# Performance work log

Hardware: AMD Instinct MI355X
Metric: run time of the kernel (lower is better)

## Reference

```python
import jax, jax.numpy as jnp
import numpy as np

N_NODES = 50000
N_EDGES = 800000
D_IN = 512
D_OUT = 512


def setup_inputs() -> dict:
    key = jax.random.key(0)
    k1, k2, k3, k4, k5 = jax.random.split(key, 5)
    adj_rows = jnp.sort(jax.random.randint(k1, (N_EDGES,), 0, N_NODES, dtype=jnp.int32))
    adj_cols = jax.random.randint(k2, (N_EDGES,), 0, N_NODES, dtype=jnp.int32)
    adj_vals = jax.random.uniform(k3, (N_EDGES,), dtype=jnp.float32)
    u_f = jax.random.normal(k4, (N_NODES, D_IN), dtype=jnp.float32)
    # xavier_uniform init for weight [in_feats, out_feats]
    limit = float(np.sqrt(6.0 / (D_IN + D_OUT)))
    weight = jax.random.uniform(k5, (D_IN, D_OUT), dtype=jnp.float32, minval=-limit, maxval=limit)
    return {"adj_rows": adj_rows, "adj_cols": adj_cols, "adj_vals": adj_vals,
            "u_f": u_f, "weight": weight}


def reference(adj_rows, adj_cols, adj_vals, u_f, weight):
    # dense projection: [N, d_in] @ [d_in, d_out] -> [N, d_out]
    h = u_f @ weight
    # sparse adj (COO) @ h: gather source rows, scale by edge vals, scatter-add to dest rows
    msgs = adj_vals[:, None] * h[adj_cols]              # [E, d_out]
    out = jax.ops.segment_sum(msgs, adj_rows, num_segments=N_NODES)  # [N, d_out]
    return jax.nn.relu(out)
```

## Files before the change

### kernel.cpp

```cpp
#include <hip/hip_runtime.h>
#include <cstdint>
#include <cstddef>

#define N_NODES 50000
#define N_EDGES 800000
#define D 512
#define M_PAD 50048

typedef __bf16 bf16x8 __attribute__((ext_vector_type(8)));
typedef float floatx4 __attribute__((ext_vector_type(4)));

typedef const __attribute__((address_space(1))) unsigned int* gas_u32p;
typedef __attribute__((address_space(3))) unsigned int* las_u32p;

__device__ __forceinline__ unsigned short f2bf(float f) {
    unsigned int u = __builtin_bit_cast(unsigned int, f);
    u += 0x7FFFu + ((u >> 16) & 1u);
    return (unsigned short)(u >> 16);
}
__device__ __forceinline__ float bflo(unsigned int u) {
    return __builtin_bit_cast(float, u << 16);
}
__device__ __forceinline__ float bfhi(unsigned int u) {
    return __builtin_bit_cast(float, u & 0xFFFF0000u);
}
__device__ __forceinline__ bf16x8 cvt8f(floatx4 lo, floatx4 hi) {
    bf16x8 r;
    r[0] = (__bf16)lo[0]; r[1] = (__bf16)lo[1]; r[2] = (__bf16)lo[2]; r[3] = (__bf16)lo[3];
    r[4] = (__bf16)hi[0]; r[5] = (__bf16)hi[1]; r[6] = (__bf16)hi[2]; r[7] = (__bf16)hi[3];
    return r;
}

__global__ __launch_bounds__(256) void k_prep(const float* __restrict__ w,
                                              unsigned short* __restrict__ wt,
                                              const int* __restrict__ rows,
                                              int* __restrict__ rp) {
    int blk = blockIdx.x;
    if (blk < 1024) {
        int id = blk * 256 + threadIdx.x;
        int n = id >> 9, k = id & 511;
        wt[id] = f2bf(w[k * D + n]);
    } else {
        int i = (blk - 1024) * 256 + threadIdx.x;
        if (i > N_NODES) return;
        int lo = 0, hi = N_EDGES;
        while (lo < hi) {
            int mid = (lo + hi) >> 1;
            if (rows[mid] < i) lo = mid + 1; else hi = mid;
        }
        rp[i] = lo;
    }
}

__global__ __launch_bounds__(256) void k_gemm(const float* __restrict__ Af,
                                              const unsigned short* __restrict__ WT,
                                              unsigned short* __restrict__ H) {
    __shared__ float          lAf[2 * 128 * 32];
    __shared__ unsigned short lB [2 * 128 * 32];
    int b = blockIdx.x;
    int mt, nt;
    if (b < 1536) {
        mt = (b >> 5) * 8 + (b & 7);
        nt = (b >> 3) & 3;
    } else {
        int r = b - 1536;
        mt = 384 + (r % 7);
        nt = r / 7;
    }
    const int tid  = threadIdx.x;
    const int wave = tid >> 6, lane = tid & 63;
    const int tileM0 = mt * 128;
    const int tileN0 = nt * 128;
    const int wr = wave >> 1, wc = wave & 1;

    const int lrowA  = lane >> 3;
    const int lslotA = lane & 7;
    int asrc[4];
#pragma unroll
    for (int g = 0; g < 4; g++) {
        int m  = wave * 32 + g * 8 + lrowA;
        int gm = tileM0 + m;
        if (gm > N_NODES - 1) gm = N_NODES - 1;
        int c = lslotA ^ (m & 7);
        asrc[g] = gm * D + c * 4;
    }

    const int lrowB = lane >> 2, lslotB = lane & 3;
    const int r0 = wave * 32;
    const int m0 = r0 + lrowB,      m1 = r0 + 16 + lrowB;
    const int q0 = (lslotB - (m0 >> 1)) & 3;
    const int q1 = (lslotB - (m1 >> 1)) & 3;
    const unsigned short* gB0 = WT + (size_t)(tileN0 + m0) * D + q0 * 8;
    const unsigned short* gB1 = WT + (size_t)(tileN0 + m1) * D + q1 * 8;

    floatx4 acc[4][4] = {};

    const int quad = lane >> 4, half = lane & 15;
    int offAlo[4], offAhi[4], offB[4];
#pragma unroll
    for (int i = 0; i < 4; i++) {
        int m = wr * 64 + i * 16 + half;
        offAlo[i] = m * 32 + (((quad * 2)     ^ (m & 7)) * 4);
        offAhi[i] = m * 32 + (((quad * 2 + 1) ^ (m & 7)) * 4);
        int n = wc * 64 + i * 16 + half;
        offB[i] = n * 32 + ((quad + (n >> 1)) & 3) * 8;
    }

    auto stage = [&](int buf, int k0) {
        float*          dA = lAf + buf * 4096;
        unsigned short* dB = lB  + buf * 4096;
#pragma unroll
        for (int g = 0; g < 4; g++)
            __builtin_amdgcn_global_load_lds((gas_u32p)(Af + asrc[g] + k0),
                                             (las_u32p)(dA + (wave * 32 + g * 8) * 32), 16, 0, 0);
        __builtin_amdgcn_global_load_lds((gas_u32p)(gB0 + k0), (las_u32p)(dB + r0 * 32), 16, 0, 0);
        __builtin_amdgcn_global_load_lds((gas_u32p)(gB1 + k0), (las_u32p)(dB + (r0 + 16) * 32), 16, 0, 0);
    };

    stage(0, 0);
    for (int kk = 0; kk < 16; kk++) {
        const int cur = kk & 1;
        if (kk < 15) {
            stage(cur ^ 1, (kk + 1) * 32);
            asm volatile("s_waitcnt vmcnt(6)" ::: "memory");
        } else {
            asm volatile("s_waitcnt vmcnt(0)" ::: "memory");
        }
        __builtin_amdgcn_s_barrier();

        const float*          cA = lAf + cur * 4096;
        const unsigned short* cB = lB  + cur * 4096;
        bf16x8 af[4], bfr[4];
#pragma unroll
        for (int i = 0; i < 4; i++) {
            floatx4 lo = *(const floatx4*)(cA + offAlo[i]);
            floatx4 hi = *(const floatx4*)(cA + offAhi[i]);
            af[i]  = cvt8f(lo, hi);
            bfr[i] = *(const bf16x8*)(cB + offB[i]);
        }
#pragma unroll
        for (int i = 0; i < 4; i++)
#pragma unroll
            for (int j = 0; j < 4; j++)
                acc[i][j] = __builtin_amdgcn_mfma_f32_16x16x32_bf16(af[i], bfr[j], acc[i][j], 0, 0, 0);

        asm volatile("s_waitcnt lgkmcnt(0)" ::: "memory");
        __builtin_amdgcn_s_barrier();
    }

#pragma unroll
    for (int i = 0; i < 4; i++) {
        int gm0 = tileM0 + wr * 64 + i * 16 + quad * 4;
#pragma unroll
        for (int j = 0; j < 4; j++) {
            int gn = tileN0 + wc * 64 + j * 16 + half;
#pragma unroll
            for (int r = 0; r < 4; r++) {
                H[(size_t)(gm0 + r) * D + gn] = f2bf(acc[i][j][r]);
            }
        }
    }
}

__global__ __launch_bounds__(256) void k_scatter(const int* __restrict__ rp,
                                                 const int* __restrict__ cols,
                                                 const float* __restrict__ vals,
                                                 const unsigned short* __restrict__ H,
                                                 float* __restrict__ out) {
    int node = (int)((blockIdx.x * 256 + threadIdx.x) >> 6);
    int lane = threadIdx.x & 63;
    if (node >= N_NODES) return;
    int s = rp[node], e = rp[node + 1];
    float a0 = 0.f, a1 = 0.f, a2 = 0.f, a3 = 0.f;
    float a4 = 0.f, a5 = 0.f, a6 = 0.f, a7 = 0.f;
    const uint4* H4 = (const uint4*)H;
    const int lq = lane;
    for (int t = s; t < e; t += 4) {
        int last = e - 1;
        int t1 = t + 1 < e ? t + 1 : last;
        int t2 = t + 2 < e ? t + 2 : last;
        int t3 = t + 3 < e ? t + 3 : last;
        int c0 = cols[t],  c1 = cols[t1], c2 = cols[t2], c3 = cols[t3];
        float v0 = vals[t];
        float v1 = t + 1 < e ? vals[t1] : 0.f;
        float v2 = t + 2 < e ? vals[t2] : 0.f;
        float v3 = t + 3 < e ? vals[t3] : 0.f;
        uint4 d0 = H4[(size_t)c0 * 64 + lq];
        uint4 d1 = H4[(size_t)c1 * 64 + lq];
        uint4 d2 = H4[(size_t)c2 * 64 + lq];
        uint4 d3 = H4[(size_t)c3 * 64 + lq];
        a0 = fmaf(v0, bflo(d0.x), a0); a1 = fmaf(v0, bfhi(d0.x), a1);
        a2 = fmaf(v0, bflo(d0.y), a2); a3 = fmaf(v0, bfhi(d0.y), a3);
        a4 = fmaf(v0, bflo(d0.z), a4); a5 = fmaf(v0, bfhi(d0.z), a5);
        a6 = fmaf(v0, bflo(d0.w), a6); a7 = fmaf(v0, bfhi(d0.w), a7);
        a0 = fmaf(v1, bflo(d1.x), a0); a1 = fmaf(v1, bfhi(d1.x), a1);
        a2 = fmaf(v1, bflo(d1.y), a2); a3 = fmaf(v1, bfhi(d1.y), a3);
        a4 = fmaf(v1, bflo(d1.z), a4); a5 = fmaf(v1, bfhi(d1.z), a5);
        a6 = fmaf(v1, bflo(d1.w), a6); a7 = fmaf(v1, bfhi(d1.w), a7);
        a0 = fmaf(v2, bflo(d2.x), a0); a1 = fmaf(v2, bfhi(d2.x), a1);
        a2 = fmaf(v2, bflo(d2.y), a2); a3 = fmaf(v2, bfhi(d2.y), a3);
        a4 = fmaf(v2, bflo(d2.z), a4); a5 = fmaf(v2, bfhi(d2.z), a5);
        a6 = fmaf(v2, bflo(d2.w), a6); a7 = fmaf(v2, bfhi(d2.w), a7);
        a0 = fmaf(v3, bflo(d3.x), a0); a1 = fmaf(v3, bfhi(d3.x), a1);
        a2 = fmaf(v3, bflo(d3.y), a2); a3 = fmaf(v3, bfhi(d3.y), a3);
        a4 = fmaf(v3, bflo(d3.z), a4); a5 = fmaf(v3, bfhi(d3.z), a5);
        a6 = fmaf(v3, bflo(d3.w), a6); a7 = fmaf(v3, bfhi(d3.w), a7);
    }
    float* o = out + (size_t)node * D + (size_t)lane * 8;
    *(float4*)o       = make_float4(fmaxf(a0, 0.f), fmaxf(a1, 0.f), fmaxf(a2, 0.f), fmaxf(a3, 0.f));
    *(float4*)(o + 4) = make_float4(fmaxf(a4, 0.f), fmaxf(a5, 0.f), fmaxf(a6, 0.f), fmaxf(a7, 0.f));
}

extern "C" void kernel_launch(void* const* d_in, const int* in_sizes, int n_in,
                              void* d_out, int out_size, void* d_ws, size_t ws_size,
                              hipStream_t stream) {
    const int*   adj_rows = (const int*)d_in[0];
    const int*   adj_cols = (const int*)d_in[1];
    const float* adj_vals = (const float*)d_in[2];
    const float* u_f      = (const float*)d_in[3];
    const float* weight   = (const float*)d_in[4];
    float* out = (float*)d_out;

    char* ws = (char*)d_ws;
    unsigned short* wt_bf = (unsigned short*)ws;
    unsigned short* h_bf  = (unsigned short*)(ws + 524288);
    int* rowptr           = (int*)(ws + 524288 + 51249152);

    hipLaunchKernelGGL(k_prep,    dim3(1220),  dim3(256), 0, stream, weight, wt_bf, adj_rows, rowptr);
    hipLaunchKernelGGL(k_gemm,    dim3(1564),  dim3(256), 0, stream, u_f, wt_bf, h_bf);
    hipLaunchKernelGGL(k_scatter, dim3(12500), dim3(256), 0, stream, rowptr, adj_cols, adj_vals, h_bf, out);
}
```

Before: 195.9 us.

## Drop LDS staging in GEMM and load MFMA fragments directly from global

The GEMM kernel no longer uses double-buffered LDS tiles filled with global_load_lds and guarded by barriers. Each wave now loads its A (fp32) and B (bf16) MFMA fragments straight from global memory every k-step and converts A to bf16 in registers. This removes LDS traffic, barriers and waitcnt synchronisation. In exchange, data shared between waves of a block is fetched redundantly through the caches, and without software prefetch there is less overlap of load latency with MFMA work.

```diff
diff --git a/kernel.cpp b/kernel.cpp
--- a/kernel.cpp
+++ b/kernel.cpp
@@ -9,9 +9,6 @@
 
 typedef __bf16 bf16x8 __attribute__((ext_vector_type(8)));
 typedef float floatx4 __attribute__((ext_vector_type(4)));
-
-typedef const __attribute__((address_space(1))) unsigned int* gas_u32p;
-typedef __attribute__((address_space(3))) unsigned int* las_u32p;
 
 __device__ __forceinline__ unsigned short f2bf(float f) {
     unsigned int u = __builtin_bit_cast(unsigned int, f);
@@ -55,8 +52,6 @@
 __global__ __launch_bounds__(256) void k_gemm(const float* __restrict__ Af,
                                               const unsigned short* __restrict__ WT,
                                               unsigned short* __restrict__ H) {
-    __shared__ float          lAf[2 * 128 * 32];
-    __shared__ unsigned short lB [2 * 128 * 32];
     int b = blockIdx.x;
     int mt, nt;
     if (b < 1536) {
@@ -72,80 +67,40 @@
     const int tileM0 = mt * 128;
     const int tileN0 = nt * 128;
     const int wr = wave >> 1, wc = wave & 1;
+    const int quad = lane >> 4, half = lane & 15;
 
-    const int lrowA  = lane >> 3;
-    const int lslotA = lane & 7;
-    int asrc[4];
+    const float*          pA[4];
+    const unsigned short* pB[4];
 #pragma unroll
-    for (int g = 0; g < 4; g++) {
-        int m  = wave * 32 + g * 8 + lrowA;
-        int gm = tileM0 + m;
+    for (int i = 0; i < 4; i++) {
+        int gm = tileM0 + wr * 64 + i * 16 + half;
         if (gm > N_NODES - 1) gm = N_NODES - 1;
-        int c = lslotA ^ (m & 7);
-        asrc[g] = gm * D + c * 4;
+        pA[i] = Af + (size_t)gm * D + quad * 8;
+        int gn = tileN0 + wc * 64 + i * 16 + half;
+        pB[i] = WT + (size_t)gn * D + quad * 8;
     }
-
-    const int lrowB = lane >> 2, lslotB = lane & 3;
-    const int r0 = wave * 32;
-    const int m0 = r0 + lrowB,      m1 = r0 + 16 + lrowB;
-    const int q0 = (lslotB - (m0 >> 1)) & 3;
-    const int q1 = (lslotB - (m1 >> 1)) & 3;
-    const unsigned short* gB0 = WT + (size_t)(tileN0 + m0) * D + q0 * 8;
-    const unsigned short* gB1 = WT + (size_t)(tileN0 + m1) * D + q1 * 8;
 
     floatx4 acc[4][4] = {};
 
-    const int quad = lane >> 4, half = lane & 15;
-    int offAlo[4], offAhi[4], offB[4];
-#pragma unroll
-    for (int i = 0; i < 4; i++) {
-        int m = wr * 64 + i * 16 + half;
-        offAlo[i] = m * 32 + (((quad * 2)     ^ (m & 7)) * 4);
-        offAhi[i] = m * 32 + (((quad * 2 + 1) ^ (m & 7)) * 4);
-        int n = wc * 64 + i * 16 + half;
-        offB[i] = n * 32 + ((quad + (n >> 1)) & 3) * 8;
-    }
-
-    auto stage = [&](int buf, int k0) {
-        float*          dA = lAf + buf * 4096;
-        unsigned short* dB = lB  + buf * 4096;
-#pragma unroll
-        for (int g = 0; g < 4; g++)
-            __builtin_amdgcn_global_load_lds((gas_u32p)(Af + asrc[g] + k0),
-                                             (las_u32p)(dA + (wave * 32 + g * 8) * 32), 16, 0, 0);
-        __builtin_amdgcn_global_load_lds((gas_u32p)(gB0 + k0), (las_u32p)(dB + r0 * 32), 16, 0, 0);
-        __builtin_amdgcn_global_load_lds((gas_u32p)(gB1 + k0), (las_u32p)(dB + (r0 + 16) * 32), 16, 0, 0);
-    };
-
-    stage(0, 0);
-    for (int kk = 0; kk < 16; kk++) {
-        const int cur = kk & 1;
-        if (kk < 15) {
-            stage(cur ^ 1, (kk + 1) * 32);
-            asm volatile("s_waitcnt vmcnt(6)" ::: "memory");
-        } else {
-            asm volatile("s_waitcnt vmcnt(0)" ::: "memory");
-        }
-        __builtin_amdgcn_s_barrier();
-
-        const float*          cA = lAf + cur * 4096;
-        const unsigned short* cB = lB  + cur * 4096;
+    for (int k0 = 0; k0 < D; k0 += 32) {
+        floatx4 lo[4], hi[4];
         bf16x8 af[4], bfr[4];
 #pragma unroll
         for (int i = 0; i < 4; i++) {
-            floatx4 lo = *(const floatx4*)(cA + offAlo[i]);
-            floatx4 hi = *(const floatx4*)(cA + offAhi[i]);
-            af[i]  = cvt8f(lo, hi);
-            bfr[i] = *(const bf16x8*)(cB + offB[i]);
+            lo[i] = *(const floatx4*)(pA[i] + k0);
+            hi[i] = *(const floatx4*)(pA[i] + k0 + 4);
         }
+#pragma unroll
+        for (int j = 0; j < 4; j++)
+            bfr[j] = *(const bf16x8*)(pB[j] + k0);
+#pragma unroll
+        for (int i = 0; i < 4; i++)
+            af[i] = cvt8f(lo[i], hi[i]);
 #pragma unroll
         for (int i = 0; i < 4; i++)
 #pragma unroll
             for (int j = 0; j < 4; j++)
                 acc[i][j] = __builtin_amdgcn_mfma_f32_16x16x32_bf16(af[i], bfr[j], acc[i][j], 0, 0, 0);
-
-        asm volatile("s_waitcnt lgkmcnt(0)" ::: "memory");
-        __builtin_amdgcn_s_barrier();
     }
 
 #pragma unroll
```

Measured after the change: 287.9 us. 1.47x slower.

## Convert A tile to bf16 in registers before LDS store in GEMM

Applied to the files above, without the earlier changes.

The fp32 A operand is now loaded into registers, converted to bf16 and written to LDS, instead of being copied to LDS as fp32 by direct global-to-LDS loads and converted on every fragment read. This halves the LDS footprint and read traffic for A, allows launch bounds of 4 blocks per CU, and removes the conversion work from the MFMA inner loop. In exchange the A prefetch now passes through VGPRs, adding register pressure and explicit waits before each store. Synchronisation also drops to one barrier per k-step.

```diff
diff --git a/kernel.cpp b/kernel.cpp
--- a/kernel.cpp
+++ b/kernel.cpp
@@ -24,10 +24,10 @@
 __device__ __forceinline__ float bfhi(unsigned int u) {
     return __builtin_bit_cast(float, u & 0xFFFF0000u);
 }
-__device__ __forceinline__ bf16x8 cvt8f(floatx4 lo, floatx4 hi) {
-    bf16x8 r;
-    r[0] = (__bf16)lo[0]; r[1] = (__bf16)lo[1]; r[2] = (__bf16)lo[2]; r[3] = (__bf16)lo[3];
-    r[4] = (__bf16)hi[0]; r[5] = (__bf16)hi[1]; r[6] = (__bf16)hi[2]; r[7] = (__bf16)hi[3];
+__device__ __forceinline__ uint2 cvt4(float4 v) {
+    uint2 r;
+    r.x = (unsigned)f2bf(v.x) | ((unsigned)f2bf(v.y) << 16);
+    r.y = (unsigned)f2bf(v.z) | ((unsigned)f2bf(v.w) << 16);
     return r;
 }
 
@@ -52,11 +52,11 @@
     }
 }
 
-__global__ __launch_bounds__(256) void k_gemm(const float* __restrict__ Af,
-                                              const unsigned short* __restrict__ WT,
-                                              unsigned short* __restrict__ H) {
-    __shared__ float          lAf[2 * 128 * 32];
-    __shared__ unsigned short lB [2 * 128 * 32];
+__global__ __launch_bounds__(256, 4) void k_gemm(const float* __restrict__ Af,
+                                                 const unsigned short* __restrict__ WT,
+                                                 unsigned short* __restrict__ H) {
+    __shared__ unsigned short lA[2 * 128 * 32];
+    __shared__ unsigned short lB[2 * 128 * 32];
     int b = blockIdx.x;
     int mt, nt;
     if (b < 1536) {
@@ -72,17 +72,18 @@
     const int tileM0 = mt * 128;
     const int tileN0 = nt * 128;
     const int wr = wave >> 1, wc = wave & 1;
-
-    const int lrowA  = lane >> 3;
-    const int lslotA = lane & 7;
-    int asrc[4];
+    const int quad = lane >> 4, half = lane & 15;
+
+    const int lrowA = lane >> 3;
+    const int q     = lane & 7;
+    int asrcR[4], wdst[4];
 #pragma unroll
     for (int g = 0; g < 4; g++) {
         int m  = wave * 32 + g * 8 + lrowA;
         int gm = tileM0 + m;
         if (gm > N_NODES - 1) gm = N_NODES - 1;
-        int c = lslotA ^ (m & 7);
-        asrc[g] = gm * D + c * 4;
+        asrcR[g] = gm * D + q * 4;
+        wdst[g]  = m * 32 + (((q >> 1) ^ ((m >> 1) & 3)) * 8) + (q & 1) * 4;
     }
 
     const int lrowB = lane >> 2, lslotB = lane & 3;
@@ -95,47 +96,46 @@
 
     floatx4 acc[4][4] = {};
 
-    const int quad = lane >> 4, half = lane & 15;
-    int offAlo[4], offAhi[4], offB[4];
+    int offA[4], offB[4];
 #pragma unroll
     for (int i = 0; i < 4; i++) {
         int m = wr * 64 + i * 16 + half;
-        offAlo[i] = m * 32 + (((quad * 2)     ^ (m & 7)) * 4);
-        offAhi[i] = m * 32 + (((quad * 2 + 1) ^ (m & 7)) * 4);
+        offA[i] = m * 32 + ((quad ^ ((half >> 1) & 3)) * 8);
         int n = wc * 64 + i * 16 + half;
         offB[i] = n * 32 + ((quad + (n >> 1)) & 3) * 8;
     }
 
-    auto stage = [&](int buf, int k0) {
-        float*          dA = lAf + buf * 4096;
-        unsigned short* dB = lB  + buf * 4096;
-#pragma unroll
-        for (int g = 0; g < 4; g++)
-            __builtin_amdgcn_global_load_lds((gas_u32p)(Af + asrc[g] + k0),
-                                             (las_u32p)(dA + (wave * 32 + g * 8) * 32), 16, 0, 0);
+    auto stageB = [&](int buf, int k0) {
+        unsigned short* dB = lB + buf * 4096;
         __builtin_amdgcn_global_load_lds((gas_u32p)(gB0 + k0), (las_u32p)(dB + r0 * 32), 16, 0, 0);
         __builtin_amdgcn_global_load_lds((gas_u32p)(gB1 + k0), (las_u32p)(dB + (r0 + 16) * 32), 16, 0, 0);
     };
 
-    stage(0, 0);
+    float4 st[4];
+#pragma unroll
+    for (int g = 0; g < 4; g++) st[g] = *(const float4*)(Af + asrcR[g]);
+    stageB(0, 0);
+    asm volatile("s_waitcnt vmcnt(2)" ::: "memory");
+#pragma unroll
+    for (int g = 0; g < 4; g++) *(uint2*)(lA + wdst[g]) = cvt4(st[g]);
+    asm volatile("s_waitcnt vmcnt(0) lgkmcnt(0)" ::: "memory");
+    __builtin_amdgcn_s_barrier();
+
     for (int kk = 0; kk < 16; kk++) {
         const int cur = kk & 1;
         if (kk < 15) {
-            stage(cur ^ 1, (kk + 1) * 32);
-            asm volatile("s_waitcnt vmcnt(6)" ::: "memory");
-        } else {
-            asm volatile("s_waitcnt vmcnt(0)" ::: "memory");
-        }
-        __builtin_amdgcn_s_barrier();
-
-        const float*          cA = lAf + cur * 4096;
-        const unsigned short* cB = lB  + cur * 4096;
+#pragma unroll
+            for (int g = 0; g < 4; g++)
+                st[g] = *(const float4*)(Af + asrcR[g] + (kk + 1) * 32);
+            stageB(cur ^ 1, (kk + 1) * 32);
+        }
+
+        const unsigned short* cA = lA + cur * 4096;
+        const unsigned short* cB = lB + cur * 4096;
         bf16x8 af[4], bfr[4];
 #pragma unroll
         for (int i = 0; i < 4; i++) {
-            floatx4 lo = *(const floatx4*)(cA + offAlo[i]);
-            floatx4 hi = *(const floatx4*)(cA + offAhi[i]);
-            af[i]  = cvt8f(lo, hi);
+            af[i]  = *(const bf16x8*)(cA + offA[i]);
             bfr[i] = *(const bf16x8*)(cB + offB[i]);
         }
 #pragma unroll
@@ -144,8 +144,14 @@
             for (int j = 0; j < 4; j++)
                 acc[i][j] = __builtin_amdgcn_mfma_f32_16x16x32_bf16(af[i], bfr[j], acc[i][j], 0, 0, 0);
 
-        asm volatile("s_waitcnt lgkmcnt(0)" ::: "memory");
-        __builtin_amdgcn_s_barrier();
+        if (kk < 15) {
+            asm volatile("s_waitcnt vmcnt(2)" ::: "memory");
+            unsigned short* dA = lA + (cur ^ 1) * 4096;
+#pragma unroll
+            for (int g = 0; g < 4; g++) *(uint2*)(dA + wdst[g]) = cvt4(st[g]);
+            asm volatile("s_waitcnt vmcnt(0) lgkmcnt(0)" ::: "memory");
+            __builtin_amdgcn_s_barrier();
+        }
     }
 
 #pragma unroll
```

Result: no change. 193.2 us (-1.4%).
